# Optimization experiments

Hardware: AMD Instinct MI355X
Metric: run time of the kernel (lower is better)

## Reference

```python
import jax, jax.numpy as jnp
import numpy as np

B, L, C = 8, 8192, 512

def setup_inputs() -> dict:
    key = jax.random.key(0)
    kq, kk, kv_, kw = jax.random.split(key, 4)
    q = jax.random.normal(kq, (B, L, C), dtype=jnp.float32)
    k = jax.random.normal(kk, (B, L, C), dtype=jnp.float32)
    v = jax.random.normal(kv_, (B, L, C), dtype=jnp.float32)
    W = jax.random.normal(kw, (C, C), dtype=jnp.float32) * (1.0 / np.sqrt(C))
    b = jnp.zeros((C,), dtype=jnp.float32)
    return {"q": q, "k": k, "v": v, "W": W, "b": b}

def reference(q, k, v, W, b):
    # L2-normalize q and k over channel dim (matches torch x / x.norm(dim=-1, keepdim=True))
    qn = q / jnp.linalg.norm(q, axis=-1, keepdims=True)
    kn = k / jnp.linalg.norm(k, axis=-1, keepdims=True)
    # kv = k * v, dropout is identity (p=0 / eval); global sum over sequence
    kv_sum = jnp.sum(kn * v, axis=-2, keepdims=True)  # [B, 1, C]
    out = kv_sum * qn                                  # [B, L, C]
    # output Linear: out @ W^T + b (torch nn.Linear convention, W:[out,in])
    return jnp.einsum('blc,oc->blo', out, W) + b
```

## Files before the change

kernel.cpp:

```cpp
#include <hip/hip_runtime.h>
#include <hip/hip_bf16.h>
#include <stdint.h>

#define B_ 8
#define L_ 8192
#define C_ 512

typedef short bf16x8 __attribute__((ext_vector_type(8)));
typedef float f32x4 __attribute__((ext_vector_type(4)));

#define GAS(p) ((const __attribute__((address_space(1))) void*)(p))
#define LAS(p) ((__attribute__((address_space(3))) void*)(p))

__global__ __launch_bounds__(256)
void kv_reduce(const float* __restrict__ kin, const float* __restrict__ vin,
               float* __restrict__ kv) {
    const int bi   = blockIdx.x;
    const int b    = bi >> 8;
    const int row0 = (bi & 255) * 32;
    const int lane = threadIdx.x & 63;
    const int wave = threadIdx.x >> 6;

    const f32x4* kb = (const f32x4*)(kin + ((size_t)b * L_ + row0) * C_);
    const f32x4* vb = (const f32x4*)(vin + ((size_t)b * L_ + row0) * C_);

    f32x4 acca = {0.f,0.f,0.f,0.f}, accb = {0.f,0.f,0.f,0.f};

    #pragma unroll 1
    for (int it = 0; it < 2; ++it) {
        const int r0 = wave * 8 + it * 4;
        f32x4 ka[4], kc[4], va[4], vc[4];
        #pragma unroll
        for (int j = 0; j < 4; ++j) {
            const f32x4* krow = kb + (size_t)(r0 + j) * (C_/4);
            ka[j] = __builtin_nontemporal_load(krow + lane);
            kc[j] = __builtin_nontemporal_load(krow + 64 + lane);
        }
        #pragma unroll
        for (int j = 0; j < 4; ++j) {
            const f32x4* vrow = vb + (size_t)(r0 + j) * (C_/4);
            va[j] = __builtin_nontemporal_load(vrow + lane);
            vc[j] = __builtin_nontemporal_load(vrow + 64 + lane);
        }
        float ss[4];
        #pragma unroll
        for (int j = 0; j < 4; ++j)
            ss[j] = ka[j][0]*ka[j][0] + ka[j][1]*ka[j][1] + ka[j][2]*ka[j][2] + ka[j][3]*ka[j][3]
                  + kc[j][0]*kc[j][0] + kc[j][1]*kc[j][1] + kc[j][2]*kc[j][2] + kc[j][3]*kc[j][3];
        #pragma unroll
        for (int m = 32; m >= 1; m >>= 1) {
            #pragma unroll
            for (int j = 0; j < 4; ++j) ss[j] += __shfl_xor(ss[j], m);
        }
        #pragma unroll
        for (int j = 0; j < 4; ++j) {
            const float inv = rsqrtf(ss[j]);
            #pragma unroll
            for (int x = 0; x < 4; ++x) {
                acca[x] += ka[j][x] * inv * va[j][x];
                accb[x] += kc[j][x] * inv * vc[j][x];
            }
        }
    }

    __shared__ __align__(16) float red[4][C_];
    ((f32x4*)&red[wave][0])[lane]      = acca;
    ((f32x4*)&red[wave][0])[64 + lane] = accb;
    __syncthreads();
    for (int c = threadIdx.x; c < C_; c += 256) {
        float s = red[0][c] + red[1][c] + red[2][c] + red[3][c];
        atomicAdd(&kv[b * C_ + c], s);
    }
}

__global__ __launch_bounds__(256)
void prep_w(const float* __restrict__ W, const float* __restrict__ kv,
            __hip_bfloat16* __restrict__ Wb) {
    int idx = blockIdx.x * 256 + threadIdx.x;
    int e   = idx << 2;
    int b   = e >> 18;
    int oc  = e & 0x3FFFF;
    int c   = oc & (C_ - 1);
    float4 w4 = *(const float4*)(W + oc);
    float4 s4 = *(const float4*)(kv + b * C_ + c);
    union { __hip_bfloat16 h[4]; uint2 u; } pk;
    pk.h[0] = __float2bfloat16(w4.x * s4.x);
    pk.h[1] = __float2bfloat16(w4.y * s4.y);
    pk.h[2] = __float2bfloat16(w4.z * s4.z);
    pk.h[3] = __float2bfloat16(w4.w * s4.w);
    *(uint2*)(Wb + e) = pk.u;
}

__global__ __launch_bounds__(256, 3)
void gemm_out(const float* __restrict__ qin, const __hip_bfloat16* __restrict__ Wb,
              const float* __restrict__ bias, float* __restrict__ out) {
    const int blk   = blockIdx.x;
    const int xcd   = blk & 7;
    const int local = blk >> 3;
    const int n0    = (local & 3) * 128;
    const int m0    = (xcd * 64 + (local >> 2)) * 128;
    const int b     = m0 >> 13;
    const int tid  = threadIdx.x;
    const int lane = tid & 63;
    const int wave = tid >> 6;

    __shared__ __align__(16) unsigned short As[128 * 64];
    __shared__ __align__(16) unsigned short Bs[128 * 64];
    __shared__ float s_inv[128];

    const int aj  = tid & 7;
    const int arp = tid >> 3;
    const float* qbase = qin + (size_t)m0 * C_;
    const __hip_bfloat16* WbB = Wb + ((size_t)b * C_ + n0) * C_;

    const int r16 = lane & 15;
    const int qd  = lane >> 4;
    const int wm  = wave & 1;
    const int wn  = wave >> 1;

    f32x4 acc[4][4];
    #pragma unroll
    for (int i = 0; i < 4; ++i)
        #pragma unroll
        for (int j = 0; j < 4; ++j)
            acc[i][j] = (f32x4){0.f, 0.f, 0.f, 0.f};

    float ssq[4] = {0.f, 0.f, 0.f, 0.f};

    for (int kc = 0; kc < C_; kc += 64) {
        if (kc) __syncthreads();
        #pragma unroll
        for (int i = 0; i < 4; ++i) {
            int cid = i * 256 + wave * 64 + lane;
            int n   = cid >> 3;
            int cj  = cid & 7;
            int kk  = ((cj ^ (n & 7)) << 3);
            const __hip_bfloat16* g = WbB + (size_t)n * C_ + kc + kk;
            __builtin_amdgcn_global_load_lds(GAS(g),
                LAS(&Bs[(i * 256 + wave * 64) * 8]), 16, 0, 0);
        }
        #pragma unroll
        for (int p = 0; p < 4; ++p) {
            int m = p * 32 + arp;
            const float* g = qbase + (size_t)m * C_ + kc + aj * 8;
            float4 x0 = ((const float4*)g)[0];
            float4 x1 = ((const float4*)g)[1];
            ssq[p] += x0.x*x0.x + x0.y*x0.y + x0.z*x0.z + x0.w*x0.w
                    + x1.x*x1.x + x1.y*x1.y + x1.z*x1.z + x1.w*x1.w;
            union { __hip_bfloat16 h[8]; uint4 u; } pk;
            pk.h[0] = __float2bfloat16(x0.x); pk.h[1] = __float2bfloat16(x0.y);
            pk.h[2] = __float2bfloat16(x0.z); pk.h[3] = __float2bfloat16(x0.w);
            pk.h[4] = __float2bfloat16(x1.x); pk.h[5] = __float2bfloat16(x1.y);
            pk.h[6] = __float2bfloat16(x1.z); pk.h[7] = __float2bfloat16(x1.w);
            *(uint4*)&As[m * 64 + ((aj ^ (m & 7)) << 3)] = pk.u;
        }
        __syncthreads();
        #pragma unroll
        for (int ks = 0; ks < 2; ++ks) {
            bf16x8 af[4], bfr[4];
            #pragma unroll
            for (int t = 0; t < 4; ++t) {
                int m = wm * 64 + t * 16 + r16;
                af[t]  = *(const bf16x8*)&As[m * 64 + (((ks * 4 + qd) ^ (m & 7)) << 3)];
                int n = wn * 64 + t * 16 + r16;
                bfr[t] = *(const bf16x8*)&Bs[n * 64 + (((ks * 4 + qd) ^ (n & 7)) << 3)];
            }
            #pragma unroll
            for (int mt = 0; mt < 4; ++mt)
                #pragma unroll
                for (int nt = 0; nt < 4; ++nt)
                    acc[mt][nt] = __builtin_amdgcn_mfma_f32_16x16x32_bf16(
                        af[mt], bfr[nt], acc[mt][nt], 0, 0, 0);
        }
    }

    #pragma unroll
    for (int p = 0; p < 4; ++p) {
        float s = ssq[p];
        s += __shfl_xor(s, 1);
        s += __shfl_xor(s, 2);
        s += __shfl_xor(s, 4);
        if (aj == 0) s_inv[p * 32 + arp] = rsqrtf(s);
    }
    __syncthreads();

    #pragma unroll
    for (int nt = 0; nt < 4; ++nt) {
        int col  = n0 + wn * 64 + nt * 16 + r16;
        float bv = bias[col];
        #pragma unroll
        for (int mt = 0; mt < 4; ++mt) {
            int rl = wm * 64 + mt * 16 + qd * 4;
            float4 inv4 = *(const float4*)&s_inv[rl];
            float* op = out + (size_t)(m0 + rl) * C_ + col;
            op[0]      = acc[mt][nt][0] * inv4.x + bv;
            op[C_]     = acc[mt][nt][1] * inv4.y + bv;
            op[2 * C_] = acc[mt][nt][2] * inv4.z + bv;
            op[3 * C_] = acc[mt][nt][3] * inv4.w + bv;
        }
    }
}

extern "C" void kernel_launch(void* const* d_in, const int* in_sizes, int n_in,
                              void* d_out, int out_size, void* d_ws, size_t ws_size,
                              hipStream_t stream) {
    const float* q    = (const float*)d_in[0];
    const float* k    = (const float*)d_in[1];
    const float* v    = (const float*)d_in[2];
    const float* W    = (const float*)d_in[3];
    const float* bias = (const float*)d_in[4];
    float* out = (float*)d_out;

    float* kv = (float*)d_ws;
    __hip_bfloat16* Wb = (__hip_bfloat16*)((char*)d_ws + 16384);

    hipMemsetAsync(kv, 0, B_ * C_ * sizeof(float), stream);
    kv_reduce<<<2048, 256, 0, stream>>>(k, v, kv);
    prep_w<<<2048, 256, 0, stream>>>(W, kv, Wb);
    gemm_out<<<2048, 256, 0, stream>>>(q, Wb, bias, out);
}
```

Before: 418.2 us.

## Double-buffer GEMM LDS tiles to overlap global loads with MFMA compute

Converts the gemm_out K-loop into a two-stage software pipeline with double-buffered A and B LDS tiles. The next K-chunk's q data is prefetched into registers and W goes straight to LDS via global_load_lds while the current chunk's MFMAs run, with one barrier per iteration instead of two. It aims to hide global memory latency behind compute, at the cost of twice the LDS and more registers, and lowers the occupancy hint from 3 to 2 blocks per CU.

```diff
diff --git a/kernel.cpp b/kernel.cpp
--- a/kernel.cpp
+++ b/kernel.cpp
@@ -91,7 +91,7 @@
     *(uint2*)(Wb + e) = pk.u;
 }
 
-__global__ __launch_bounds__(256, 3)
+__global__ __launch_bounds__(256, 2)
 void gemm_out(const float* __restrict__ qin, const __hip_bfloat16* __restrict__ Wb,
               const float* __restrict__ bias, float* __restrict__ out) {
     const int blk   = blockIdx.x;
@@ -104,8 +104,8 @@
     const int lane = tid & 63;
     const int wave = tid >> 6;
 
-    __shared__ __align__(16) unsigned short As[128 * 64];
-    __shared__ __align__(16) unsigned short Bs[128 * 64];
+    __shared__ __align__(16) unsigned short As[2][128 * 64];
+    __shared__ __align__(16) unsigned short Bs[2][128 * 64];
     __shared__ float s_inv[128];
 
     const int aj  = tid & 7;
@@ -126,9 +126,9 @@
             acc[i][j] = (f32x4){0.f, 0.f, 0.f, 0.f};
 
     float ssq[4] = {0.f, 0.f, 0.f, 0.f};
-
-    for (int kc = 0; kc < C_; kc += 64) {
-        if (kc) __syncthreads();
+    float4 xa[4], xb[4];
+
+    auto stageB = [&](int buf, int kc) {
         #pragma unroll
         for (int i = 0; i < 4; ++i) {
             int cid = i * 256 + wave * 64 + lane;
@@ -137,14 +137,22 @@
             int kk  = ((cj ^ (n & 7)) << 3);
             const __hip_bfloat16* g = WbB + (size_t)n * C_ + kc + kk;
             __builtin_amdgcn_global_load_lds(GAS(g),
-                LAS(&Bs[(i * 256 + wave * 64) * 8]), 16, 0, 0);
-        }
+                LAS(&Bs[buf][(i * 256 + wave * 64) * 8]), 16, 0, 0);
+        }
+    };
+    auto loadA = [&](int kc) {
+        #pragma unroll
+        for (int p = 0; p < 4; ++p) {
+            const float* g = qbase + (size_t)(p * 32 + arp) * C_ + kc + aj * 8;
+            xa[p] = ((const float4*)g)[0];
+            xb[p] = ((const float4*)g)[1];
+        }
+    };
+    auto writeA = [&](int buf) {
         #pragma unroll
         for (int p = 0; p < 4; ++p) {
             int m = p * 32 + arp;
-            const float* g = qbase + (size_t)m * C_ + kc + aj * 8;
-            float4 x0 = ((const float4*)g)[0];
-            float4 x1 = ((const float4*)g)[1];
+            float4 x0 = xa[p], x1 = xb[p];
             ssq[p] += x0.x*x0.x + x0.y*x0.y + x0.z*x0.z + x0.w*x0.w
                     + x1.x*x1.x + x1.y*x1.y + x1.z*x1.z + x1.w*x1.w;
             union { __hip_bfloat16 h[8]; uint4 u; } pk;
@@ -152,18 +160,19 @@
             pk.h[2] = __float2bfloat16(x0.z); pk.h[3] = __float2bfloat16(x0.w);
             pk.h[4] = __float2bfloat16(x1.x); pk.h[5] = __float2bfloat16(x1.y);
             pk.h[6] = __float2bfloat16(x1.z); pk.h[7] = __float2bfloat16(x1.w);
-            *(uint4*)&As[m * 64 + ((aj ^ (m & 7)) << 3)] = pk.u;
-        }
-        __syncthreads();
+            *(uint4*)&As[buf][m * 64 + ((aj ^ (m & 7)) << 3)] = pk.u;
+        }
+    };
+    auto compute = [&](int buf) {
         #pragma unroll
         for (int ks = 0; ks < 2; ++ks) {
             bf16x8 af[4], bfr[4];
             #pragma unroll
             for (int t = 0; t < 4; ++t) {
                 int m = wm * 64 + t * 16 + r16;
-                af[t]  = *(const bf16x8*)&As[m * 64 + (((ks * 4 + qd) ^ (m & 7)) << 3)];
+                af[t]  = *(const bf16x8*)&As[buf][m * 64 + (((ks * 4 + qd) ^ (m & 7)) << 3)];
                 int n = wn * 64 + t * 16 + r16;
-                bfr[t] = *(const bf16x8*)&Bs[n * 64 + (((ks * 4 + qd) ^ (n & 7)) << 3)];
+                bfr[t] = *(const bf16x8*)&Bs[buf][n * 64 + (((ks * 4 + qd) ^ (n & 7)) << 3)];
             }
             #pragma unroll
             for (int mt = 0; mt < 4; ++mt)
@@ -172,7 +181,23 @@
                     acc[mt][nt] = __builtin_amdgcn_mfma_f32_16x16x32_bf16(
                         af[mt], bfr[nt], acc[mt][nt], 0, 0, 0);
         }
-    }
+    };
+
+    stageB(0, 0);
+    loadA(0);
+    writeA(0);
+    __syncthreads();
+
+    #pragma unroll
+    for (int t = 0; t < 7; ++t) {
+        const int cur = t & 1, nxt = cur ^ 1;
+        stageB(nxt, (t + 1) * 64);
+        loadA((t + 1) * 64);
+        compute(cur);
+        writeA(nxt);
+        __syncthreads();
+    }
+    compute(1);
 
     #pragma unroll
     for (int p = 0; p < 4; ++p) {
```

After: 473.4 us. 1.13x slower.
